# Kernel tuning notes

Hardware: AMD Instinct MI355X
Metric: run time of the kernel (lower is better)

## Reference

```python
import jax, jax.numpy as jnp
import numpy as np

N_NODES = 20000
N_EDGES = 640000
BASIS = 128
NUM_GAUSS = 64
HIDDEN = 256
NUM_ATOMS = 100
NUM_GRAPHS = 256
T = 3


def setup_inputs() -> dict:
    key = jax.random.key(0)
    ks = jax.random.split(key, 16)
    Z = jax.random.randint(ks[0], (N_NODES,), 0, NUM_ATOMS + 1)
    edge_index = jax.random.randint(ks[1], (2, N_EDGES), 0, N_NODES)
    edge_attr = jax.random.normal(ks[2], (N_EDGES, NUM_GAUSS), dtype=jnp.float32)
    batch = jnp.sort(jax.random.randint(ks[3], (N_NODES,), 0, NUM_GRAPHS))
    s = 0.05
    embed = jax.random.normal(ks[4], (NUM_ATOMS + 1, BASIS), dtype=jnp.float32)
    cfW = jax.random.normal(ks[5], (BASIS, BASIS), dtype=jnp.float32) * s
    cfb = jax.random.normal(ks[6], (BASIS,), dtype=jnp.float32) * s
    dfW = jax.random.normal(ks[7], (BASIS, NUM_GAUSS), dtype=jnp.float32) * s
    dfb = jax.random.normal(ks[8], (BASIS,), dtype=jnp.float32) * s
    fcW = jax.random.normal(ks[9], (BASIS, BASIS), dtype=jnp.float32) * s
    r1W = jax.random.normal(ks[10], (HIDDEN, BASIS), dtype=jnp.float32) * s
    r1b = jax.random.normal(ks[11], (HIDDEN,), dtype=jnp.float32) * s
    r2W = jax.random.normal(ks[12], (4, HIDDEN), dtype=jnp.float32) * s
    r2b = jax.random.normal(ks[13], (4,), dtype=jnp.float32) * s
    return dict(Z=Z, edge_index=edge_index, edge_attr=edge_attr, batch=batch,
                embed=embed, cfW=cfW, cfb=cfb, dfW=dfW, dfb=dfb, fcW=fcW,
                r1W=r1W, r1b=r1b, r2W=r2W, r2b=r2b)


def reference(Z, edge_index, edge_attr, batch, embed, cfW, cfb, dfW, dfb, fcW,
              r1W, r1b, r2W, r2b):
    # Node embeddings C: [N, basis]
    C = embed[Z]
    src = edge_index[0]  # x_j source nodes
    dst = edge_index[1]  # aggregation target nodes
    # df(edge_attr) is iteration-invariant (shared InteractionBlock weights)
    d_feat = edge_attr @ dfW.T + dfb  # [E, basis]
    for _ in range(T):
        # message: tanh(fc(cf(x_j) * df(edge_attr)))
        c_feat = C[src] @ cfW.T + cfb                 # [E, basis]
        m = jnp.tanh((c_feat * d_feat) @ fcW.T)       # [E, basis]
        agg = jax.ops.segment_sum(m, dst, num_segments=N_NODES)
        C = C + agg
    # readout MLP: Linear -> tanh -> Linear
    h = jnp.tanh(C @ r1W.T + r1b) @ r2W.T + r2b       # [N, 4]
    # global_add_pool over graphs
    return jax.ops.segment_sum(h, batch, num_segments=NUM_GRAPHS)  # [G, 4]
```

## Files before the change

### kernel.cpp

```cpp
#include <hip/hip_runtime.h>
#include <cstdint>

#define NN 20000
#define NE 640000
#define NB 128
#define NG 64
#define NH 256

typedef __attribute__((ext_vector_type(8))) short bf16x8;
typedef __attribute__((ext_vector_type(4))) float f32x4;
typedef __attribute__((ext_vector_type(4))) float fvec4;
typedef __attribute__((ext_vector_type(4))) unsigned uvec4;

__device__ __forceinline__ unsigned fbits(float f){ union{float f; unsigned u;} v; v.f=f; return v.u; }
__device__ __forceinline__ float ubits(unsigned u){ union{unsigned u; float f;} v; v.u=u; return v.f; }

__device__ __forceinline__ unsigned pkf(float a, float b){
  return __builtin_amdgcn_perm(fbits(b)+0x8000u, fbits(a)+0x8000u, 0x07060302u);
}
__device__ __forceinline__ unsigned mulbb(unsigned c, unsigned d){
  float lo = ubits(c << 16) * ubits(d << 16);
  float hi = ubits(c & 0xFFFF0000u) * ubits(d & 0xFFFF0000u);
  return pkf(lo, hi);
}
__device__ __forceinline__ short f2bf_fast(float f){ return (short)((fbits(f)+0x8000u)>>16); }

__device__ __forceinline__ float tanh_fast(float x){
  float t = __builtin_amdgcn_exp2f(x * 2.8853900817779268f);
  return __builtin_fmaf(-2.f, __builtin_amdgcn_rcpf(t + 1.f), 1.f);
}

template<int NT, int KT>
__device__ __forceinline__ void stage_w(const float* __restrict__ W, short* lds){
  const int total = NT*KT*64;
  for(int c = (int)threadIdx.x; c < total; c += 256){
    int lane = c & 63;
    int kt = (c >> 6) % KT;
    int n  = c / (64*KT);
    int row = n*16 + (lane & 15);
    int col = kt*32 + (lane >> 4)*8;
    const float* p = W + (size_t)row*(KT*32) + col;
    unsigned* d = (unsigned*)(lds + (size_t)c*8);
#pragma unroll
    for(int j=0;j<4;j++) d[j] = pkf(p[2*j], p[2*j+1]);
  }
}

__global__ void k_prep0(const int* __restrict__ Z, const float* __restrict__ E,
                        float* __restrict__ C, const int* __restrict__ dst, int* __restrict__ cnt){
  int i = blockIdx.x*256 + threadIdx.x;
  int node = i >> 5, k4 = i & 31;
  ((float4*)C)[i] = ((const float4*)(E + (size_t)Z[node]*NB))[k4];
  atomicAdd(&cnt[dst[i]], 1);
}

__global__ __launch_bounds__(1024) void k_scan(const int* __restrict__ cnt, int* __restrict__ cur){
  __shared__ int lds[1024];
  const int t = threadIdx.x;
  const int base = t*20;
  int4 v[5];
#pragma unroll
  for(int j=0;j<5;j++) v[j] = ((const int4*)(cnt + base))[j];
  const int* ve = (const int*)v;
  int loc[20]; int s = 0;
#pragma unroll
  for(int j=0;j<20;j++){ int c = (base+j < NN) ? ve[j] : 0; loc[j] = s; s += c; }
  lds[t] = s;
  __syncthreads();
  for(int off=1; off<1024; off<<=1){
    int x = (t >= off) ? lds[t-off] : 0;
    __syncthreads();
    lds[t] += x;
    __syncthreads();
  }
  int prefix = (t > 0) ? lds[t-1] : 0;
#pragma unroll
  for(int j=0;j<20;j++){ int i = base+j; if(i<NN) cur[i] = prefix + loc[j]; }
}

__global__ void k_fill(const int* __restrict__ src, const int* __restrict__ dst,
                       int* __restrict__ cur, int* __restrict__ perm,
                       int* __restrict__ srcv, int* __restrict__ dstv){
  int e = blockIdx.x*256 + threadIdx.x;
  if(e < NE){
    int v = dst[e];
    int p = atomicAdd(&cur[v], 1);
    perm[p] = e;
    srcv[p] = src[e];
    dstv[p] = v;
  }
}

#define TPAD 136
__global__ __launch_bounds__(256,3) void k_dprep(
  const float* __restrict__ ea, const int* __restrict__ perm,
  const float* __restrict__ dfW, const float* __restrict__ dfb, short* __restrict__ dft)
{
  __shared__ short ldsW[8*2*64*8];
  __shared__ short ldsT[4*32*TPAD];
  stage_w<8,2>(dfW, ldsW);
  __syncthreads();
  const int lane = threadIdx.x & 63, wave = threadIdx.x >> 6;
  const int quad = lane>>4, lc = lane&15;
  short* myT = ldsT + wave*32*TPAD;
  const int wid = blockIdx.x*4 + wave;
#pragma unroll 1
  for(int tile = wid; tile < NN; tile += 3072){
    const int base = tile*32;
    bf16x8 a[2][2];
#pragma unroll
    for(int mt=0;mt<2;mt++){
      int e = perm[base + mt*16 + lc];
      const float* p = ea + (size_t)e*NG;
#pragma unroll
      for(int kt=0;kt<2;kt++){
        const float* q = p + kt*32 + quad*8;
        fvec4 c0 = __builtin_nontemporal_load((const fvec4*)q);
        fvec4 c1 = __builtin_nontemporal_load((const fvec4*)(q+4));
        union{ bf16x8 v; unsigned u[4]; } t;
        t.u[0]=pkf(c0.x,c0.y); t.u[1]=pkf(c0.z,c0.w); t.u[2]=pkf(c1.x,c1.y); t.u[3]=pkf(c1.z,c1.w);
        a[mt][kt] = t.v;
      }
    }
    f32x4 acc[2][8];
    f32x4 z = {0.f,0.f,0.f,0.f};
#pragma unroll
    for(int mt=0;mt<2;mt++)
#pragma unroll
      for(int n2=0;n2<8;n2++) acc[mt][n2] = z;
#pragma unroll
    for(int kt=0;kt<2;kt++)
#pragma unroll
      for(int n2=0;n2<8;n2++){
        bf16x8 b = *(const bf16x8*)(ldsW + ((size_t)(n2*2+kt)*64 + lane)*8);
        acc[0][n2] = __builtin_amdgcn_mfma_f32_16x16x32_bf16(a[0][kt], b, acc[0][n2], 0, 0, 0);
        acc[1][n2] = __builtin_amdgcn_mfma_f32_16x16x32_bf16(a[1][kt], b, acc[1][n2], 0, 0, 0);
      }
#pragma unroll
    for(int n2=0;n2<8;n2++){
      float bias = dfb[n2*16 + lc];
#pragma unroll
      for(int mt=0;mt<2;mt++)
#pragma unroll
        for(int r=0;r<4;r++)
          myT[(mt*16 + quad*4 + r)*TPAD + n2*16 + lc] = f2bf_fast(acc[mt][n2][r] + bias);
    }
    short* gout = dft + (size_t)base*NB;
#pragma unroll
    for(int i=0;i<8;i++){
      int s_ = i*512 + lane*8;
      int row = s_ >> 7, col = s_ & 127;
      uvec4 vv = *(const uvec4*)(myT + row*TPAD + col);
      __builtin_nontemporal_store(vv, (uvec4*)(gout + s_));
    }
  }
}

__global__ __launch_bounds__(256,3) void k_cf(
  const float* __restrict__ C, const float* __restrict__ cfW,
  const float* __restrict__ cfb, short* __restrict__ cfC)
{
  __shared__ short ldsW[8*4*64*8];
  __shared__ short ldsT[4*16*TPAD];
  stage_w<8,4>(cfW, ldsW);
  __syncthreads();
  const int lane = threadIdx.x & 63, wave = threadIdx.x >> 6;
  const int quad = lane>>4, lc = lane&15;
  short* myT = ldsT + wave*16*TPAD;
  const int tile = blockIdx.x*4 + wave;
  if(tile >= NN/16) return;
  const int base = tile*16;
  bf16x8 a[4];
  const float* p = C + (size_t)(base + lc)*NB;
#pragma unroll
  for(int kt=0;kt<4;kt++){
    const float* q = p + kt*32 + quad*8;
    float4 c0 = *(const float4*)q, c1 = *(const float4*)(q+4);
    union{ bf16x8 v; unsigned u[4]; } t;
    t.u[0]=pkf(c0.x,c0.y); t.u[1]=pkf(c0.z,c0.w); t.u[2]=pkf(c1.x,c1.y); t.u[3]=pkf(c1.z,c1.w);
    a[kt] = t.v;
  }
  f32x4 acc[8];
  f32x4 z = {0.f,0.f,0.f,0.f};
#pragma unroll
  for(int n2=0;n2<8;n2++) acc[n2] = z;
#pragma unroll
  for(int kt=0;kt<4;kt++)
#pragma unroll
    for(int n2=0;n2<8;n2++){
      bf16x8 b = *(const bf16x8*)(ldsW + ((size_t)(n2*4+kt)*64 + lane)*8);
      acc[n2] = __builtin_amdgcn_mfma_f32_16x16x32_bf16(a[kt], b, acc[n2], 0, 0, 0);
    }
#pragma unroll
  for(int n2=0;n2<8;n2++){
    float bias = cfb[n2*16 + lc];
#pragma unroll
    for(int r=0;r<4;r++)
      myT[(quad*4 + r)*TPAD + n2*16 + lc] = f2bf_fast(acc[n2][r] + bias);
  }
  short* gout = cfC + (size_t)base*NB;
#pragma unroll
  for(int i=0;i<4;i++){
    int s_ = i*512 + lane*8;
    int row = s_ >> 7, col = s_ & 127;
    uint4 vv = *(const uint4*)(myT + row*TPAD + col);
    *(uint4*)(gout + s_) = vv;
  }
}

__global__ __launch_bounds__(256,2) void k_edge(
    const short* __restrict__ cfC, const short* __restrict__ dft,
    const int* __restrict__ srcv, const int* __restrict__ dstv,
    const float* __restrict__ fcW, float* __restrict__ C)
{
  __shared__ short ldsW[8*4*64*8];
  stage_w<8,4>(fcW, ldsW);
  __syncthreads();
  const int lane = threadIdx.x & 63, wave = threadIdx.x >> 6;
  const int quad = lane>>4, lc = lane&15;
  const int tile0 = (blockIdx.x*4 + wave)*2;
#pragma unroll 1
  for(int s = 0; s < 2; s++){
    const int base = (tile0 + s)*32;
    bf16x8 a2[2][4];
#pragma unroll
    for(int mt=0; mt<2; mt++){
      const int e = base + mt*16 + lc;
      const short* cp = cfC + (size_t)srcv[e]*NB;
      const short* dp = dft + (size_t)e*NB;
#pragma unroll
      for(int kt=0; kt<4; kt++){
        uint4 cc = *(const uint4*)(cp + kt*32 + quad*8);
        uint4 dd = *(const uint4*)(dp + kt*32 + quad*8);
        union{ bf16x8 v; unsigned u[4]; } t;
        t.u[0] = mulbb(cc.x, dd.x);
        t.u[1] = mulbb(cc.y, dd.y);
        t.u[2] = mulbb(cc.z, dd.z);
        t.u[3] = mulbb(cc.w, dd.w);
        a2[mt][kt] = t.v;
      }
    }
    f32x4 acc[2][8];
    f32x4 z = {0.f,0.f,0.f,0.f};
#pragma unroll
    for(int mt=0;mt<2;mt++)
#pragma unroll
      for(int n2=0;n2<8;n2++) acc[mt][n2] = z;
#pragma unroll
    for(int kt=0; kt<4; kt++)
#pragma unroll
      for(int n2=0; n2<8; n2++){
        bf16x8 b = *(const bf16x8*)(ldsW + ((size_t)(n2*4 + kt)*64 + lane)*8);
        acc[0][n2] = __builtin_amdgcn_mfma_f32_16x16x32_bf16(a2[0][kt], b, acc[0][n2], 0, 0, 0);
        acc[1][n2] = __builtin_amdgcn_mfma_f32_16x16x32_bf16(a2[1][kt], b, acc[1][n2], 0, 0, 0);
      }
#pragma unroll
    for(int mt=0;mt<2;mt++)
#pragma unroll
      for(int n2=0;n2<8;n2++)
#pragma unroll
        for(int r=0;r<4;r++) acc[mt][n2][r] = tanh_fast(acc[mt][n2][r]);

    const int i = lane & 31;
    const int di = dstv[base + i];
    const int dprev = (i > 0) ? dstv[base + i - 1] : -1;
    unsigned long long mm = __ballot(di != dprev) & 0xFFFFFFFFull;
    while(mm){
      int lo = __ffsll(mm) - 1;
      mm &= mm - 1;
      int hi = mm ? (__ffsll(mm) - 1) : 32;
      int v = __shfl(di, lo);
      float sums[8];
#pragma unroll
      for(int n2=0;n2<8;n2++) sums[n2] = 0.f;
#pragma unroll
      for(int mt=0; mt<2; mt++)
#pragma unroll
        for(int r=0; r<4; r++){
          int e2 = mt*16 + quad*4 + r;
          float sel = (e2 >= lo && e2 < hi) ? 1.f : 0.f;
#pragma unroll
          for(int n2=0;n2<8;n2++) sums[n2] = __builtin_fmaf(acc[mt][n2][r], sel, sums[n2]);
        }
#pragma unroll
      for(int n2=0;n2<8;n2++){
        sums[n2] += __shfl_xor(sums[n2], 16);
        sums[n2] += __shfl_xor(sums[n2], 32);
      }
      const int n2w = quad*2;
      atomicAdd(&C[(size_t)v*NB + n2w*16 + lc],     sums[n2w]);
      atomicAdd(&C[(size_t)v*NB + (n2w+1)*16 + lc], sums[n2w+1]);
    }
  }
}

__global__ __launch_bounds__(256,2) void k_readout(
  const float* __restrict__ C, const float* __restrict__ r1W, const float* __restrict__ r1b,
  const float* __restrict__ r2W, const float* __restrict__ r2b,
  const int* __restrict__ batch, float* __restrict__ out)
{
  __shared__ short ldsW[16*4*64*8];
  stage_w<16,4>(r1W, ldsW);
  __syncthreads();
  const int lane = threadIdx.x & 63, wave = threadIdx.x >> 6;
  const int quad = lane>>4, lc = lane&15;
  const int base = (blockIdx.x*4 + wave)*16;
  if(base >= NN) return;
  int node = base + lc; if(node > NN-1) node = NN-1;
  bf16x8 a[4];
  const float* p = C + (size_t)node*NB;
#pragma unroll
  for(int kt=0;kt<4;kt++){
    const float* q = p + kt*32 + quad*8;
    float4 c0 = *(const float4*)q, c1 = *(const float4*)(q+4);
    union{ bf16x8 v; unsigned u[4]; } t;
    t.u[0]=pkf(c0.x,c0.y); t.u[1]=pkf(c0.z,c0.w); t.u[2]=pkf(c1.x,c1.y); t.u[3]=pkf(c1.z,c1.w);
    a[kt] = t.v;
  }
  f32x4 acc[16];
  f32x4 z = {0.f,0.f,0.f,0.f};
#pragma unroll
  for(int nt=0;nt<16;nt++) acc[nt] = z;
#pragma unroll
  for(int kt=0;kt<4;kt++)
#pragma unroll
    for(int nt=0;nt<16;nt++){
      bf16x8 b = *(const bf16x8*)(ldsW + ((size_t)(nt*4+kt)*64 + lane)*8);
      acc[nt] = __builtin_amdgcn_mfma_f32_16x16x32_bf16(a[kt], b, acc[nt], 0, 0, 0);
    }
#pragma unroll
  for(int nt=0;nt<16;nt++){
    float bias = r1b[nt*16 + lc];
#pragma unroll
    for(int r=0;r<4;r++) acc[nt][r] = tanh_fast(acc[nt][r] + bias);
  }
#pragma unroll
  for(int r=0;r<4;r++){
    int nd = base + quad*4 + r;
#pragma unroll
    for(int o=0;o<4;o++){
      float ps = 0.f;
#pragma unroll
      for(int nt=0;nt<16;nt++) ps = __builtin_fmaf(acc[nt][r], r2W[(size_t)o*NH + nt*16 + lc], ps);
      ps += __shfl_xor(ps, 1);
      ps += __shfl_xor(ps, 2);
      ps += __shfl_xor(ps, 4);
      ps += __shfl_xor(ps, 8);
      if(lc == 0 && nd < NN) atomicAdd(&out[batch[nd]*4 + o], ps + r2b[o]);
    }
  }
}

extern "C" void kernel_launch(void* const* d_in, const int* in_sizes, int n_in,
                              void* d_out, int out_size, void* d_ws, size_t ws_size,
                              hipStream_t stream) {
  const int*   Z      = (const int*)d_in[0];
  const int*   ei     = (const int*)d_in[1];
  const float* ea     = (const float*)d_in[2];
  const int*   batch  = (const int*)d_in[3];
  const float* embedW = (const float*)d_in[4];
  const float* cfW    = (const float*)d_in[5];
  const float* cfb    = (const float*)d_in[6];
  const float* dfW    = (const float*)d_in[7];
  const float* dfb    = (const float*)d_in[8];
  const float* fcW    = (const float*)d_in[9];
  const float* r1W    = (const float*)d_in[10];
  const float* r1b    = (const float*)d_in[11];
  const float* r2W    = (const float*)d_in[12];
  const float* r2b    = (const float*)d_in[13];
  const int* src = ei;
  const int* dst = ei + NE;

  char* p = (char*)d_ws;
  auto alloc = [&](size_t b){ char* r = p; p += (b + 255) & ~(size_t)255; return r; };
  float* CA    = (float*)alloc((size_t)NN*NB*4);
  short* cfC   = (short*)alloc((size_t)NN*NB*2);
  short* dft   = (short*)alloc((size_t)NE*NB*2);
  int*   cnt   = (int*)alloc((size_t)NN*4);
  int*   cursor= (int*)alloc((size_t)NN*4);
  int*   perm  = (int*)alloc((size_t)NE*4);
  int*   srcv  = (int*)alloc((size_t)NE*4);
  int*   dstv  = (int*)alloc((size_t)NE*4);
  size_t needed = (size_t)(p - (char*)d_ws);

  (void)hipMemsetAsync(d_out, 0, (size_t)out_size*sizeof(float), stream);
  if(needed > ws_size) return;

  (void)hipMemsetAsync(cnt, 0, (size_t)NN*4, stream);
  k_prep0<<<2500, 256, 0, stream>>>(Z, embedW, CA, dst, cnt);
  k_scan <<<1,   1024, 0, stream>>>(cnt, cursor);
  k_fill <<<2500, 256, 0, stream>>>(src, dst, cursor, perm, srcv, dstv);
  k_dprep<<<768,  256, 0, stream>>>(ea, perm, dfW, dfb, dft);

  for(int it = 0; it < 3; it++){
    k_cf  <<<313,  256, 0, stream>>>(CA, cfW, cfb, cfC);
    k_edge<<<2500, 256, 0, stream>>>(cfC, dft, srcv, dstv, fcW, CA);
  }
  k_readout<<<313, 256, 0, stream>>>(CA, r1W, r1b, r2W, r2b, batch, (float*)d_out);
}
```

Measured before the change: 716.4 us.

## Software-pipeline edge and dprep kernels with register double-buffered prefetch

k_edge now handles four 32-edge tiles per wave and double-buffers the src/dst indices, dft rows and gathered cfC rows in registers. The next tile's loads are issued before and during the current tile's MFMA work. dst indices are loaded once per tile and the previous value comes from a shuffle instead of a second global load. k_dprep drops its grid-stride loop for two tiles per wave, prefetching the second tile's edge attributes while the first is computed and stored, with the launch grid enlarged to match. This should hide gather latency but raises register pressure, which could reduce occupancy.

```diff
diff --git a/kernel.cpp b/kernel.cpp
--- a/kernel.cpp
+++ b/kernel.cpp
@@ -103,49 +103,67 @@
   const int lane = threadIdx.x & 63, wave = threadIdx.x >> 6;
   const int quad = lane>>4, lc = lane&15;
   short* myT = ldsT + wave*32*TPAD;
-  const int wid = blockIdx.x*4 + wave;
-#pragma unroll 1
-  for(int tile = wid; tile < NN; tile += 3072){
-    const int base = tile*32;
-    bf16x8 a[2][2];
-#pragma unroll
-    for(int mt=0;mt<2;mt++){
-      int e = perm[base + mt*16 + lc];
-      const float* p = ea + (size_t)e*NG;
-#pragma unroll
-      for(int kt=0;kt<2;kt++){
-        const float* q = p + kt*32 + quad*8;
-        fvec4 c0 = __builtin_nontemporal_load((const fvec4*)q);
-        fvec4 c1 = __builtin_nontemporal_load((const fvec4*)(q+4));
-        union{ bf16x8 v; unsigned u[4]; } t;
-        t.u[0]=pkf(c0.x,c0.y); t.u[1]=pkf(c0.z,c0.w); t.u[2]=pkf(c1.x,c1.y); t.u[3]=pkf(c1.z,c1.w);
-        a[mt][kt] = t.v;
-      }
-    }
-    f32x4 acc[2][8];
-    f32x4 z = {0.f,0.f,0.f,0.f};
+  const int tile0 = (blockIdx.x*4 + wave)*2;
+
+  float bias[8];
+#pragma unroll
+  for(int n2=0;n2<8;n2++) bias[n2] = dfb[n2*16 + lc];
+
+  int eA[2], eB[2];
+#pragma unroll
+  for(int mt=0;mt<2;mt++){
+    eA[mt] = perm[ tile0   *32 + mt*16 + lc];
+    eB[mt] = perm[(tile0+1)*32 + mt*16 + lc];
+  }
+
+  fvec4 rA[2][2][2];
+#pragma unroll
+  for(int mt=0;mt<2;mt++){
+    const float* p = ea + (size_t)eA[mt]*NG;
+#pragma unroll
+    for(int kt=0;kt<2;kt++){
+      const float* q = p + kt*32 + quad*8;
+      rA[mt][kt][0] = __builtin_nontemporal_load((const fvec4*)q);
+      rA[mt][kt][1] = __builtin_nontemporal_load((const fvec4*)(q+4));
+    }
+  }
+
+  f32x4 z = {0.f,0.f,0.f,0.f};
+
+  auto convert_mfma = [&](fvec4 (&raw)[2][2][2], f32x4 (&acc)[2][8]){
 #pragma unroll
     for(int mt=0;mt<2;mt++)
 #pragma unroll
       for(int n2=0;n2<8;n2++) acc[mt][n2] = z;
 #pragma unroll
-    for(int kt=0;kt<2;kt++)
+    for(int kt=0;kt<2;kt++){
+      bf16x8 a0, a1;
+      {
+        union{ bf16x8 v; unsigned u[4]; } t0, t1;
+        fvec4 c0 = raw[0][kt][0], c1 = raw[0][kt][1];
+        fvec4 d0 = raw[1][kt][0], d1 = raw[1][kt][1];
+        t0.u[0]=pkf(c0.x,c0.y); t0.u[1]=pkf(c0.z,c0.w); t0.u[2]=pkf(c1.x,c1.y); t0.u[3]=pkf(c1.z,c1.w);
+        t1.u[0]=pkf(d0.x,d0.y); t1.u[1]=pkf(d0.z,d0.w); t1.u[2]=pkf(d1.x,d1.y); t1.u[3]=pkf(d1.z,d1.w);
+        a0 = t0.v; a1 = t1.v;
+      }
 #pragma unroll
       for(int n2=0;n2<8;n2++){
         bf16x8 b = *(const bf16x8*)(ldsW + ((size_t)(n2*2+kt)*64 + lane)*8);
-        acc[0][n2] = __builtin_amdgcn_mfma_f32_16x16x32_bf16(a[0][kt], b, acc[0][n2], 0, 0, 0);
-        acc[1][n2] = __builtin_amdgcn_mfma_f32_16x16x32_bf16(a[1][kt], b, acc[1][n2], 0, 0, 0);
-      }
-#pragma unroll
-    for(int n2=0;n2<8;n2++){
-      float bias = dfb[n2*16 + lc];
+        acc[0][n2] = __builtin_amdgcn_mfma_f32_16x16x32_bf16(a0, b, acc[0][n2], 0, 0, 0);
+        acc[1][n2] = __builtin_amdgcn_mfma_f32_16x16x32_bf16(a1, b, acc[1][n2], 0, 0, 0);
+      }
+    }
+  };
+
+  auto store_tile = [&](f32x4 (&acc)[2][8], int tile){
+#pragma unroll
+    for(int n2=0;n2<8;n2++)
 #pragma unroll
       for(int mt=0;mt<2;mt++)
 #pragma unroll
         for(int r=0;r<4;r++)
-          myT[(mt*16 + quad*4 + r)*TPAD + n2*16 + lc] = f2bf_fast(acc[mt][n2][r] + bias);
-    }
-    short* gout = dft + (size_t)base*NB;
+          myT[(mt*16 + quad*4 + r)*TPAD + n2*16 + lc] = f2bf_fast(acc[mt][n2][r] + bias[n2]);
+    short* gout = dft + (size_t)tile*32*NB;
 #pragma unroll
     for(int i=0;i<8;i++){
       int s_ = i*512 + lane*8;
@@ -153,7 +171,28 @@
       uvec4 vv = *(const uvec4*)(myT + row*TPAD + col);
       __builtin_nontemporal_store(vv, (uvec4*)(gout + s_));
     }
-  }
+  };
+
+  f32x4 accA[2][8];
+  convert_mfma(rA, accA);
+
+  fvec4 rB[2][2][2];
+#pragma unroll
+  for(int mt=0;mt<2;mt++){
+    const float* p = ea + (size_t)eB[mt]*NG;
+#pragma unroll
+    for(int kt=0;kt<2;kt++){
+      const float* q = p + kt*32 + quad*8;
+      rB[mt][kt][0] = __builtin_nontemporal_load((const fvec4*)q);
+      rB[mt][kt][1] = __builtin_nontemporal_load((const fvec4*)(q+4));
+    }
+  }
+
+  store_tile(accA, tile0);
+
+  f32x4 accB[2][8];
+  convert_mfma(rB, accB);
+  store_tile(accB, tile0+1);
 }
 
 __global__ __launch_bounds__(256,3) void k_cf(
@@ -208,6 +247,7 @@
   }
 }
 
+#define ETPW 4
 __global__ __launch_bounds__(256,2) void k_edge(
     const short* __restrict__ cfC, const short* __restrict__ dft,
     const int* __restrict__ srcv, const int* __restrict__ dstv,
@@ -218,28 +258,49 @@
   __syncthreads();
   const int lane = threadIdx.x & 63, wave = threadIdx.x >> 6;
   const int quad = lane>>4, lc = lane&15;
-  const int tile0 = (blockIdx.x*4 + wave)*2;
-#pragma unroll 1
-  for(int s = 0; s < 2; s++){
-    const int base = (tile0 + s)*32;
-    bf16x8 a2[2][4];
-#pragma unroll
-    for(int mt=0; mt<2; mt++){
-      const int e = base + mt*16 + lc;
-      const short* cp = cfC + (size_t)srcv[e]*NB;
-      const short* dp = dft + (size_t)e*NB;
-#pragma unroll
-      for(int kt=0; kt<4; kt++){
-        uint4 cc = *(const uint4*)(cp + kt*32 + quad*8);
-        uint4 dd = *(const uint4*)(dp + kt*32 + quad*8);
-        union{ bf16x8 v; unsigned u[4]; } t;
-        t.u[0] = mulbb(cc.x, dd.x);
-        t.u[1] = mulbb(cc.y, dd.y);
-        t.u[2] = mulbb(cc.z, dd.z);
-        t.u[3] = mulbb(cc.w, dd.w);
-        a2[mt][kt] = t.v;
-      }
-    }
+  const int tile0 = (blockIdx.x*4 + wave)*ETPW;
+
+  int   sv[2][2];
+  int   dv[2];
+  uint4 cc[2][2][4];
+  uint4 dd[2][2][4];
+
+  {
+    const int base = tile0*32;
+#pragma unroll
+    for(int mt=0;mt<2;mt++) sv[0][mt] = srcv[base + mt*16 + lc];
+    dv[0] = dstv[base + (lane&31)];
+#pragma unroll
+    for(int mt=0;mt<2;mt++){
+      const short* dp = dft + (size_t)(base + mt*16 + lc)*NB;
+#pragma unroll
+      for(int kt=0;kt<4;kt++) dd[0][mt][kt] = *(const uint4*)(dp + kt*32 + quad*8);
+    }
+#pragma unroll
+    for(int mt=0;mt<2;mt++){
+      const short* cp = cfC + (size_t)sv[0][mt]*NB;
+#pragma unroll
+      for(int kt=0;kt<4;kt++) cc[0][mt][kt] = *(const uint4*)(cp + kt*32 + quad*8);
+    }
+  }
+
+#pragma unroll
+  for(int t=0; t<ETPW; t++){
+    const int cur = t & 1, nxt = cur ^ 1;
+
+    if(t+1 < ETPW){
+      const int nbase = (tile0 + t + 1)*32;
+#pragma unroll
+      for(int mt=0;mt<2;mt++) sv[nxt][mt] = srcv[nbase + mt*16 + lc];
+      dv[nxt] = dstv[nbase + (lane&31)];
+#pragma unroll
+      for(int mt=0;mt<2;mt++){
+        const short* dp = dft + (size_t)(nbase + mt*16 + lc)*NB;
+#pragma unroll
+        for(int kt=0;kt<4;kt++) dd[nxt][mt][kt] = *(const uint4*)(dp + kt*32 + quad*8);
+      }
+    }
+
     f32x4 acc[2][8];
     f32x4 z = {0.f,0.f,0.f,0.f};
 #pragma unroll
@@ -247,13 +308,35 @@
 #pragma unroll
       for(int n2=0;n2<8;n2++) acc[mt][n2] = z;
 #pragma unroll
-    for(int kt=0; kt<4; kt++)
-#pragma unroll
-      for(int n2=0; n2<8; n2++){
+    for(int kt=0;kt<4;kt++){
+      bf16x8 a0, a1;
+      {
+        union{ bf16x8 v; unsigned u[4]; } t0, t1;
+        uint4 c0 = cc[cur][0][kt], d0 = dd[cur][0][kt];
+        uint4 c1 = cc[cur][1][kt], d1 = dd[cur][1][kt];
+        t0.u[0] = mulbb(c0.x, d0.x); t0.u[1] = mulbb(c0.y, d0.y);
+        t0.u[2] = mulbb(c0.z, d0.z); t0.u[3] = mulbb(c0.w, d0.w);
+        t1.u[0] = mulbb(c1.x, d1.x); t1.u[1] = mulbb(c1.y, d1.y);
+        t1.u[2] = mulbb(c1.z, d1.z); t1.u[3] = mulbb(c1.w, d1.w);
+        a0 = t0.v; a1 = t1.v;
+      }
+#pragma unroll
+      for(int n2=0;n2<8;n2++){
         bf16x8 b = *(const bf16x8*)(ldsW + ((size_t)(n2*4 + kt)*64 + lane)*8);
-        acc[0][n2] = __builtin_amdgcn_mfma_f32_16x16x32_bf16(a2[0][kt], b, acc[0][n2], 0, 0, 0);
-        acc[1][n2] = __builtin_amdgcn_mfma_f32_16x16x32_bf16(a2[1][kt], b, acc[1][n2], 0, 0, 0);
-      }
+        acc[0][n2] = __builtin_amdgcn_mfma_f32_16x16x32_bf16(a0, b, acc[0][n2], 0, 0, 0);
+        acc[1][n2] = __builtin_amdgcn_mfma_f32_16x16x32_bf16(a1, b, acc[1][n2], 0, 0, 0);
+      }
+    }
+
+    if(t+1 < ETPW){
+#pragma unroll
+      for(int mt=0;mt<2;mt++){
+        const short* cp = cfC + (size_t)sv[nxt][mt]*NB;
+#pragma unroll
+        for(int kt=0;kt<4;kt++) cc[nxt][mt][kt] = *(const uint4*)(cp + kt*32 + quad*8);
+      }
+    }
+
 #pragma unroll
     for(int mt=0;mt<2;mt++)
 #pragma unroll
@@ -262,8 +345,9 @@
         for(int r=0;r<4;r++) acc[mt][n2][r] = tanh_fast(acc[mt][n2][r]);
 
     const int i = lane & 31;
-    const int di = dstv[base + i];
-    const int dprev = (i > 0) ? dstv[base + i - 1] : -1;
+    const int di = dv[cur];
+    const int dshift = __shfl_up(di, 1);
+    const int dprev = (i > 0) ? dshift : -1;
     unsigned long long mm = __ballot(di != dprev) & 0xFFFFFFFFull;
     while(mm){
       int lo = __ffsll(mm) - 1;
@@ -390,11 +474,11 @@
   k_prep0<<<2500, 256, 0, stream>>>(Z, embedW, CA, dst, cnt);
   k_scan <<<1,   1024, 0, stream>>>(cnt, cursor);
   k_fill <<<2500, 256, 0, stream>>>(src, dst, cursor, perm, srcv, dstv);
-  k_dprep<<<768,  256, 0, stream>>>(ea, perm, dfW, dfb, dft);
+  k_dprep<<<2500, 256, 0, stream>>>(ea, perm, dfW, dfb, dft);
 
   for(int it = 0; it < 3; it++){
     k_cf  <<<313,  256, 0, stream>>>(CA, cfW, cfb, cfC);
-    k_edge<<<2500, 256, 0, stream>>>(cfC, dft, srcv, dstv, fcW, CA);
+    k_edge<<<1250, 256, 0, stream>>>(cfC, dft, srcv, dstv, fcW, CA);
   }
   k_readout<<<313, 256, 0, stream>>>(CA, r1W, r1b, r2W, r2b, batch, (float*)d_out);
 }
```

After: 666.1 us. 7.0% less time.
